# Kernel optimization log

Measured on AMD Instinct MI355X. Metric: run time of the kernel, lower is better.

The kernel has to match this reference:

```python
import jax, jax.numpy as jnp
import numpy as np

B, S, IN, OUT = 4, 2048, 4096, 1024
ROUNDS = 12  # prime_factors(4096) == [2]*12
QMIN, QMAX = -128, 127


def _create_noise(key, shape, lo, hi):
    # Obfuscation noise spanning the data range; exactly corrected in forward.
    return jax.random.uniform(key, shape, jnp.float32, -0.5, 0.5) * (hi - lo)


def setup_inputs() -> dict:
    key = jax.random.key(0)
    ks = jax.random.split(key, 6)
    x = jax.random.normal(ks[0], (B, S, IN), jnp.float32)
    weight = jax.random.normal(ks[1], (OUT, IN), jnp.float32) * 0.02
    bias = jax.random.normal(ks[2], (OUT,), jnp.float32) * 0.02
    weight_noise = _create_noise(ks[3], (OUT, IN), weight.min(), weight.max())
    noise_x = _create_noise(ks[4], (B, S, IN), x.min(), x.max())
    # one random permutation of in_features per round
    perms = jnp.stack([jax.random.permutation(jax.random.fold_in(key, 1000 + r), IN)
                       for r in range(ROUNDS)]).astype(jnp.int32)
    # 2048 random orthogonal 2x2 blocks per round (rotations, like ortho_group with dim=2)
    theta = jax.random.uniform(ks[5], (ROUNDS, IN // 2), jnp.float32, 0.0, 2.0 * np.pi)
    c, s = jnp.cos(theta), jnp.sin(theta)
    row0 = jnp.stack([c, -s], axis=-1)
    row1 = jnp.stack([s, c], axis=-1)
    matrices = jnp.stack([row0, row1], axis=-2)  # (ROUNDS, IN//2, 2, 2)
    return {"x": x, "weight": weight, "bias": bias, "weight_noise": weight_noise,
            "noise_x": noise_x, "permutations": perms, "matrices": matrices}


def _permute_matrix_operation(X, perms, mats):
    # X: (..., n, cols). Each round: gather rows by permutation, then apply a
    # block-diagonal orthogonal transform (G blocks of size f along the n axis).
    lead = X.shape[:-2]
    n, cols = X.shape[-2], X.shape[-1]
    G, f = mats.shape[1], mats.shape[2]
    for r in range(mats.shape[0]):
        X = jnp.take(X, perms[r], axis=-2)
        Xb = X.reshape(lead + (G, f, cols))
        X = jnp.einsum('gij,...gjc->...gic', mats[r], Xb).reshape(lead + (n, cols))
    return X


def _quant_dequant(t):
    # Asymmetric per-tensor quantize -> round -> clamp -> dequantize (int8-style).
    lo, hi = t.min(), t.max()
    scale = (hi - lo) / (QMAX - QMIN)
    zp = jnp.round(QMIN - lo / scale)
    q = jnp.clip(jnp.round(t / scale + zp), QMIN, QMAX)
    return (q - zp) * scale


def reference(x, weight, bias, weight_noise, noise_x, permutations, matrices):
    # inverse-transpose blocks; equals `matrices` for orthogonal blocks, kept explicit for fidelity
    inv_mats_mT = jnp.swapaxes(jnp.linalg.inv(matrices), -1, -2)
    w_plus = weight + weight_noise                                   # (OUT, IN)
    permuted_w = jnp.swapaxes(
        _permute_matrix_operation(jnp.swapaxes(w_plus, -1, -2), permutations, inv_mats_mT), -1, -2)
    qw = _quant_dequant(permuted_w)                                  # (OUT, IN)
    permuted_x = jnp.swapaxes(
        _permute_matrix_operation(jnp.swapaxes(x + noise_x, -1, -2), permutations, matrices), -1, -2)
    qx = _quant_dequant(permuted_x)                                  # (B, S, IN)
    res = qx @ qw.T + bias                                           # quantized matmul + bias
    res = res - x @ weight_noise.T                                   # correction term 1
    res = res - noise_x @ w_plus.T                                   # correction term 2
    return res
```

## Files before the change

### kernel.cpp

```cpp
#include <hip/hip_runtime.h>


#define IN_F   4096
#define OUT_F  1024
#define MROWS  8192
#define KTOT   12288
#define KHALF  6144
#define NPASS  6
#define NTIL   96

typedef _Float16 f16;
typedef _Float16 f16x8 __attribute__((ext_vector_type(8)));
typedef _Float16 f16x4 __attribute__((ext_vector_type(4)));
typedef float    f32x4 __attribute__((ext_vector_type(4)));

#define OFF_XT  (0ull)
#define OFF_WT  (OFF_XT + (size_t)MROWS * IN_F * 4)
#define OFF_A   (OFF_WT + (size_t)OUT_F * IN_F * 4)
#define OFF_B   (OFF_A + (size_t)MROWS * KTOT * 2)
#define OFF_MM  (OFF_B + (size_t)OUT_F * KTOT * 2)
#define OFF_TIX (OFF_MM + 256)
#define OFF_TCX (OFF_TIX + (size_t)NPASS * 2048 * 8)
#define OFF_TIW (OFF_TCX + (size_t)NPASS * 2048 * 32)
#define OFF_TCW (OFF_TIW + (size_t)NPASS * 2048 * 8)

__device__ __forceinline__ unsigned enc_f(float f) {
  unsigned u = __float_as_uint(f);
  return (u & 0x80000000u) ? ~u : (u | 0x80000000u);
}
__device__ __forceinline__ float dec_f(unsigned u) {
  unsigned b = (u & 0x80000000u) ? (u & 0x7fffffffu) : ~u;
  return __uint_as_float(b);
}

__global__ void build_tables_kernel(const int* __restrict__ perms,
                                    const float* __restrict__ mats,
                                    uint2* __restrict__ tIx, float4* __restrict__ tCx,
                                    uint2* __restrict__ tIw, float4* __restrict__ tCw,
                                    unsigned* __restrict__ mm) {
  if (blockIdx.x == 0 && threadIdx.x == 0) {
    mm[0] = 0xFFFFFFFFu; mm[1] = 0u; mm[2] = 0xFFFFFFFFu; mm[3] = 0u;
  }
  int p = blockIdx.x;
  int r0 = 2 * p, r1 = 2 * p + 1;
  for (int g = threadIdx.x; g < 2048; g += blockDim.x) {
    int q0 = perms[r1 * IN_F + 2 * g], q1 = perms[r1 * IN_F + 2 * g + 1];
    int a0 = q0 >> 1, e0 = q0 & 1, a1 = q1 >> 1, e1 = q1 & 1;
    unsigned i0 = perms[r0 * IN_F + 2 * a0], i1 = perms[r0 * IN_F + 2 * a0 + 1];
    unsigned i2 = perms[r0 * IN_F + 2 * a1], i3 = perms[r0 * IN_F + 2 * a1 + 1];
    uint2 idx = make_uint2(i0 | (i1 << 16), i2 | (i3 << 16));
    const float* Ma = mats + ((size_t)r0 * 2048 + a0) * 4;
    const float* Mb = mats + ((size_t)r0 * 2048 + a1) * 4;
    const float* M1 = mats + ((size_t)r1 * 2048 + g) * 4;
    int o = p * 2048 + g;
    {
      float c00 = Ma[e0 * 2], c01 = Ma[e0 * 2 + 1];
      float c10 = Mb[e1 * 2], c11 = Mb[e1 * 2 + 1];
      float m00 = M1[0], m01 = M1[1], m10 = M1[2], m11 = M1[3];
      tIx[o] = idx;
      tCx[2 * o]     = make_float4(m00 * c00, m00 * c01, m01 * c10, m01 * c11);
      tCx[2 * o + 1] = make_float4(m10 * c00, m10 * c01, m11 * c10, m11 * c11);
    }
    {
      float rda = 1.0f / (Ma[0] * Ma[3] - Ma[1] * Ma[2]);
      float rdb = 1.0f / (Mb[0] * Mb[3] - Mb[1] * Mb[2]);
      float rd1 = 1.0f / (M1[0] * M1[3] - M1[1] * M1[2]);
      float c00 = (e0 == 0 ? Ma[3] : -Ma[1]) * rda;
      float c01 = (e0 == 0 ? -Ma[2] : Ma[0]) * rda;
      float c10 = (e1 == 0 ? Mb[3] : -Mb[1]) * rdb;
      float c11 = (e1 == 0 ? -Mb[2] : Mb[0]) * rdb;
      float m00 = M1[3] * rd1, m01 = -M1[2] * rd1;
      float m10 = -M1[1] * rd1, m11 = M1[0] * rd1;
      tIw[o] = idx;
      tCw[2 * o]     = make_float4(m00 * c00, m00 * c01, m01 * c10, m01 * c11);
      tCw[2 * o + 1] = make_float4(m10 * c00, m10 * c01, m11 * c10, m11 * c11);
    }
  }
}

__global__ __launch_bounds__(1024) void transform_kernel(
    const float* __restrict__ x, const float* __restrict__ nx,
    const float* __restrict__ w, const float* __restrict__ wn,
    const uint2* __restrict__ tIx, const float4* __restrict__ tCx,
    const uint2* __restrict__ tIw, const float4* __restrict__ tCw,
    float* __restrict__ xt, float* __restrict__ wt,
    f16* __restrict__ Aall, f16* __restrict__ Ball,
    unsigned* __restrict__ mm) {
  __shared__ float2 buf[2][IN_F];
  const int t = threadIdx.x;
  const bool isW = blockIdx.x >= (MROWS / 2);
  const float *in0, *in1; const uint2* tI; const float4* tC;
  float* tout; f16* fout; int mmidx; size_t m0;
  if (!isW) {
    m0 = (size_t)blockIdx.x * 2;
    in0 = x; in1 = nx; tI = tIx; tC = tCx; tout = xt; fout = Aall; mmidx = 0;
  } else {
    m0 = (size_t)(blockIdx.x - MROWS / 2) * 2;
    in0 = w; in1 = wn; tI = tIw; tC = tCw; tout = wt; fout = Ball; mmidx = 2;
  }
  f16* f0 = fout + m0 * KTOT;
  f16* f1 = fout + (m0 + 1) * KTOT;

  {
    float4 a0 = ((const float4*)(in0 + m0 * IN_F))[t];
    float4 b0 = ((const float4*)(in1 + m0 * IN_F))[t];
    float4 a1 = ((const float4*)(in0 + (m0 + 1) * IN_F))[t];
    float4 b1 = ((const float4*)(in1 + (m0 + 1) * IN_F))[t];
    float4 s0 = make_float4(a0.x + b0.x, a0.y + b0.y, a0.z + b0.z, a0.w + b0.w);
    float4 s1 = make_float4(a1.x + b1.x, a1.y + b1.y, a1.z + b1.z, a1.w + b1.w);
    int c = t * 4;
    *(float4*)&buf[0][c]     = make_float4(s0.x, s1.x, s0.y, s1.y);
    *(float4*)&buf[0][c + 2] = make_float4(s0.z, s1.z, s0.w, s1.w);
    f16x4 p0, p1, q0, q1;
    if (isW) {
      p0.x=(f16)b0.x; p0.y=(f16)b0.y; p0.z=(f16)b0.z; p0.w=(f16)b0.w;
      q0.x=(f16)s0.x; q0.y=(f16)s0.y; q0.z=(f16)s0.z; q0.w=(f16)s0.w;
      p1.x=(f16)b1.x; p1.y=(f16)b1.y; p1.z=(f16)b1.z; p1.w=(f16)b1.w;
      q1.x=(f16)s1.x; q1.y=(f16)s1.y; q1.z=(f16)s1.z; q1.w=(f16)s1.w;
    } else {
      p0.x=(f16)(-a0.x); p0.y=(f16)(-a0.y); p0.z=(f16)(-a0.z); p0.w=(f16)(-a0.w);
      q0.x=(f16)(-b0.x); q0.y=(f16)(-b0.y); q0.z=(f16)(-b0.z); q0.w=(f16)(-b0.w);
      p1.x=(f16)(-a1.x); p1.y=(f16)(-a1.y); p1.z=(f16)(-a1.z); p1.w=(f16)(-a1.w);
      q1.x=(f16)(-b1.x); q1.y=(f16)(-b1.y); q1.z=(f16)(-b1.z); q1.w=(f16)(-b1.w);
    }
    *(f16x4*)(f0 + IN_F + c)     = p0;
    *(f16x4*)(f0 + 2 * IN_F + c) = q0;
    *(f16x4*)(f1 + IN_F + c)     = p1;
    *(f16x4*)(f1 + 2 * IN_F + c) = q1;
  }
  __syncthreads();

  int cur = 0;
  for (int pass = 0; pass < NPASS; pass++) {
    const uint2* ti = tI + pass * 2048;
    const float4* tc = tC + (size_t)pass * 4096;
#pragma unroll
    for (int i = 0; i < 2; i++) {
      int g = i * 1024 + t;
      uint2 pk = ti[g];
      float4 cA = tc[2 * g], cB = tc[2 * g + 1];
      float2 x0 = buf[cur][pk.x & 0xffff], x1 = buf[cur][pk.x >> 16];
      float2 x2 = buf[cur][pk.y & 0xffff], x3 = buf[cur][pk.y >> 16];
      float y0x = cA.x * x0.x + cA.y * x1.x + cA.z * x2.x + cA.w * x3.x;
      float y0y = cA.x * x0.y + cA.y * x1.y + cA.z * x2.y + cA.w * x3.y;
      float y1x = cB.x * x0.x + cB.y * x1.x + cB.z * x2.x + cB.w * x3.x;
      float y1y = cB.x * x0.y + cB.y * x1.y + cB.z * x2.y + cB.w * x3.y;
      *(float4*)&buf[cur ^ 1][2 * g] = make_float4(y0x, y0y, y1x, y1y);
    }
    cur ^= 1;
    __syncthreads();
  }
  float lmin = 3.4e38f, lmax = -3.4e38f;
  {
    int c = t * 4;
    float4 q0 = *(float4*)&buf[0][c];
    float4 q1 = *(float4*)&buf[0][c + 2];
    ((float4*)(tout + m0 * IN_F))[t]       = make_float4(q0.x, q0.z, q1.x, q1.z);
    ((float4*)(tout + (m0 + 1) * IN_F))[t] = make_float4(q0.y, q0.w, q1.y, q1.w);
    lmin = fminf(fminf(fminf(q0.x, q0.y), fminf(q0.z, q0.w)),
                 fminf(fminf(q1.x, q1.y), fminf(q1.z, q1.w)));
    lmax = fmaxf(fmaxf(fmaxf(q0.x, q0.y), fmaxf(q0.z, q0.w)),
                 fmaxf(fmaxf(q1.x, q1.y), fmaxf(q1.z, q1.w)));
  }
#pragma unroll
  for (int off = 32; off > 0; off >>= 1) {
    lmin = fminf(lmin, __shfl_down(lmin, off));
    lmax = fmaxf(lmax, __shfl_down(lmax, off));
  }
  float* red = (float*)&buf[1][0];
  int wid = t >> 6;
  if ((t & 63) == 0) { red[wid * 2] = lmin; red[wid * 2 + 1] = lmax; }
  __syncthreads();
  if (t == 0) {
    float bmin = red[0], bmax = red[1];
#pragma unroll
    for (int i = 1; i < 16; i++) {
      bmin = fminf(bmin, red[i * 2]);
      bmax = fmaxf(bmax, red[i * 2 + 1]);
    }
    atomicMin(&mm[mmidx], enc_f(bmin));
    atomicMax(&mm[mmidx + 1], enc_f(bmax));
  }
}

__global__ void finalize_kernel(unsigned* mm) {
  float* sc = (float*)(mm + 4);
  float xlo = dec_f(mm[0]), xhi = dec_f(mm[1]);
  float wlo = dec_f(mm[2]), whi = dec_f(mm[3]);
  float sx = (xhi - xlo) / 255.0f;
  float zx = rintf(-128.0f - xlo / sx);
  float sw = (whi - wlo) / 255.0f;
  float zw = rintf(-128.0f - wlo / sw);
  sc[0] = sx; sc[1] = zx; sc[2] = sw; sc[3] = zw;
}

__global__ __launch_bounds__(256) void quant_kernel(
    const float* __restrict__ xt, const float* __restrict__ wt,
    f16* __restrict__ Aall, f16* __restrict__ Ball,
    const unsigned* __restrict__ mm) {
  const float* sc = (const float*)(mm + 4);
  const bool isW = blockIdx.x >= MROWS;
  int m = isW ? blockIdx.x - MROWS : blockIdx.x;
  float s = isW ? sc[2] : sc[0], zp = isW ? sc[3] : sc[1];
  const float4* srow = (const float4*)((isW ? wt : xt) + (size_t)m * IN_F);
  f16* drow = (isW ? Ball : Aall) + (size_t)m * KTOT;
  int t = threadIdx.x;
#pragma unroll
  for (int j = 0; j < 4; j++) {
    int i4 = j * 256 + t;
    float4 v = srow[i4];
    float q0 = (fminf(fmaxf(rintf(v.x / s + zp), -128.f), 127.f) - zp) * s;
    float q1 = (fminf(fmaxf(rintf(v.y / s + zp), -128.f), 127.f) - zp) * s;
    float q2 = (fminf(fmaxf(rintf(v.z / s + zp), -128.f), 127.f) - zp) * s;
    float q3 = (fminf(fmaxf(rintf(v.w / s + zp), -128.f), 127.f) - zp) * s;
    f16x4 o; o.x = (f16)q0; o.y = (f16)q1; o.z = (f16)q2; o.w = (f16)q3;
    *(f16x4*)(drow + i4 * 4) = o;
  }
}

__global__ __launch_bounds__(256) void bias_init_kernel(
    const float* __restrict__ bias, float* __restrict__ out) {
  const float4* b4 = (const float4*)bias;
  float4* o4 = (float4*)out;
  int idx = blockIdx.x * 256 + threadIdx.x;
  const int total = MROWS * OUT_F / 4;
  for (int i = idx; i < total; i += gridDim.x * 256)
    o4[i] = b4[i & (OUT_F / 4 - 1)];
}

__device__ __forceinline__ void gl2lds16(const void* g, void* l) {
  __builtin_amdgcn_global_load_lds(
      (__attribute__((address_space(1))) void*)g,
      (__attribute__((address_space(3))) void*)l, 16, 0, 0);
}

#define GBAR() asm volatile("s_barrier" ::: "memory")
#define MFMA16(d, va, vb) d = __builtin_amdgcn_mfma_f32_16x16x32_f16(va, vb, d, 0, 0, 0)

#define STAGE(t, hh) do {                                                   \
    const int c_ = (t) & 1;                                                 \
    if ((hh) < 2) {                                                         \
      const f16* g_ = gA + (size_t)((hh) * 128) * KTOT + (size_t)(t) * 64;  \
      f16* l_ = As + c_ * 16384 + (hh) * 8192 + sbase;                      \
      gl2lds16(g_, l_);                                                     \
      gl2lds16(g_ + (size_t)64 * KTOT, l_ + 4096);                          \
    } else {                                                                \
      const f16* g_ = gB + (size_t)(((hh) - 2) * 128) * KTOT + (size_t)(t) * 64; \
      f16* l_ = Bs + c_ * 16384 + ((hh) - 2) * 8192 + sbase;                \
      gl2lds16(g_, l_);                                                     \
      gl2lds16(g_ + (size_t)64 * KTOT, l_ + 4096);                          \
    }                                                                       \
  } while (0)

__global__ __launch_bounds__(512, 2) void gemm_kernel(
    const f16* __restrict__ A, const f16* __restrict__ B,
    float* __restrict__ out) {
  extern __shared__ f16 sm[];
  f16* As = sm;
  f16* Bs = sm + 32768;

  const int tid = threadIdx.x;
  const int wave = tid >> 6, lane = tid & 63;
  const int fr = lane & 15, quad = lane >> 4;
  const int wm = wave >> 2, wn = wave & 3;

  const int orig = blockIdx.x;
  const int wg = (orig & 7) * 32 + (orig >> 3);
  const int ks = wg >> 7;
  const int rem = wg & 127;
  const int bn = rem >> 5, bm = rem & 31;
  const size_t k0 = (size_t)ks * KHALF;

  const int srow = (wave << 3) + (lane >> 3);
  const int scol = (((lane & 7) ^ (lane >> 3)) << 3);
  const f16* gA = A + ((size_t)bm * 256 + srow) * KTOT + k0 + scol;
  const f16* gB = B + ((size_t)bn * 256 + srow) * KTOT + k0 + scol;
  const int sbase = wave << 9;

  const int co0 = ((quad ^ (fr & 7)) << 3);
  const int co1 = co0 ^ 32;
  const f16* rA0 = As + wm * 8192 + fr * 64 + co0;
  const f16* rA1 = As + wm * 8192 + fr * 64 + co1;
  const f16* rB0 = Bs + (wn >> 1) * 8192 + (wn & 1) * 4096 + fr * 64 + co0;
  const f16* rB1 = Bs + (wn >> 1) * 8192 + (wn & 1) * 4096 + fr * 64 + co1;

  f16x8 a0[4][2], a1[4][2], bF[4][2];
  f32x4 acc[8][4] = {};

  STAGE(0, 0); STAGE(0, 1); STAGE(0, 2); STAGE(0, 3);
  STAGE(1, 0); STAGE(1, 1);
  asm volatile("s_waitcnt vmcnt(4)" ::: "memory");
  GBAR();

  for (int t = 0; t < NTIL; ++t) {
    const int c = t & 1;
    const f16* pa0 = rA0 + c * 16384;
    const f16* pa1 = rA1 + c * 16384;
    const f16* pb0 = rB0 + c * 16384;
    const f16* pb1 = rB1 + c * 16384;

#pragma unroll
    for (int i = 0; i < 4; i++) {
      a0[i][0] = *(const f16x8*)(pa0 + i * 1024);
      a0[i][1] = *(const f16x8*)(pa1 + i * 1024);
    }
#pragma unroll
    for (int j = 0; j < 2; j++) {
      bF[j][0] = *(const f16x8*)(pb0 + j * 1024);
      bF[j][1] = *(const f16x8*)(pb1 + j * 1024);
    }
    if (t + 1 < NTIL) STAGE(t + 1, 2);
    GBAR();
    __builtin_amdgcn_s_setprio(1);
#pragma unroll
    for (int i = 0; i < 4; i++)
#pragma unroll
      for (int j = 0; j < 2; j++) {
        MFMA16(acc[i][j], a0[i][0], bF[j][0]);
        MFMA16(acc[i][j], a0[i][1], bF[j][1]);
      }
    __builtin_amdgcn_s_setprio(0);
    GBAR();

#pragma unroll
    for (int i = 0; i < 4; i++) {
      a1[i][0] = *(const f16x8*)(pa0 + (4 + i) * 1024);
      a1[i][1] = *(const f16x8*)(pa1 + (4 + i) * 1024);
    }
#pragma unroll
    for (int j = 0; j < 2; j++) {
      bF[2 + j][0] = *(const f16x8*)(pb0 + (2 + j) * 1024);
      bF[2 + j][1] = *(const f16x8*)(pb1 + (2 + j) * 1024);
    }
    if (t + 1 < NTIL) STAGE(t + 1, 3);
    GBAR();
    __builtin_amdgcn_s_setprio(1);
#pragma unroll
    for (int i = 0; i < 4; i++)
#pragma unroll
      for (int j = 0; j < 2; j++) {
        MFMA16(acc[i][2 + j], a0[i][0], bF[2 + j][0]);
        MFMA16(acc[i][2 + j], a0[i][1], bF[2 + j][1]);
      }
    __builtin_amdgcn_s_setprio(0);
    GBAR();

    if (t + 2 < NTIL) STAGE(t + 2, 0);
    GBAR();
    __builtin_amdgcn_s_setprio(1);
#pragma unroll
    for (int i = 0; i < 4; i++)
#pragma unroll
      for (int j = 0; j < 2; j++) {
        MFMA16(acc[4 + i][j], a1[i][0], bF[j][0]);
        MFMA16(acc[4 + i][j], a1[i][1], bF[j][1]);
      }
    __builtin_amdgcn_s_setprio(0);
    GBAR();

    if (t + 2 < NTIL) STAGE(t + 2, 1);
    if (t + 2 < NTIL) {
      asm volatile("s_waitcnt vmcnt(4)" ::: "memory");
    } else if (t + 1 < NTIL) {
      asm volatile("s_waitcnt vmcnt(0)" ::: "memory");
    }
    GBAR();
    __builtin_amdgcn_s_setprio(1);
#pragma unroll
    for (int i = 0; i < 4; i++)
#pragma unroll
      for (int j = 0; j < 2; j++) {
        MFMA16(acc[4 + i][2 + j], a1[i][0], bF[2 + j][0]);
        MFMA16(acc[4 + i][2 + j], a1[i][1], bF[2 + j][1]);
      }
    __builtin_amdgcn_s_setprio(0);
    GBAR();
  }

  const size_t orow = (size_t)bm * 256 + wm * 128 + quad * 4;
  const int ocol = bn * 256 + wn * 64 + fr;
#pragma unroll
  for (int mi = 0; mi < 8; mi++)
#pragma unroll
    for (int ni = 0; ni < 4; ni++)
#pragma unroll
      for (int e = 0; e < 4; e++)
        unsafeAtomicAdd(&out[(orow + mi * 16 + e) * OUT_F + (ocol + ni * 16)],
                        acc[mi][ni][e]);
}

extern "C" void kernel_launch(void* const* d_in, const int* in_sizes, int n_in,
                              void* d_out, int out_size, void* d_ws, size_t ws_size,
                              hipStream_t stream) {
  const float* x     = (const float*)d_in[0];
  const float* w     = (const float*)d_in[1];
  const float* bias  = (const float*)d_in[2];
  const float* wn    = (const float*)d_in[3];
  const float* nx    = (const float*)d_in[4];
  const int*   perms = (const int*)d_in[5];
  const float* mats  = (const float*)d_in[6];
  float* out = (float*)d_out;

  char* ws = (char*)d_ws;
  float* xt   = (float*)(ws + OFF_XT);
  float* wt   = (float*)(ws + OFF_WT);
  f16*   Aall = (f16*)(ws + OFF_A);
  f16*   Ball = (f16*)(ws + OFF_B);
  unsigned* mm = (unsigned*)(ws + OFF_MM);
  uint2*  tIx = (uint2*)(ws + OFF_TIX);
  float4* tCx = (float4*)(ws + OFF_TCX);
  uint2*  tIw = (uint2*)(ws + OFF_TIW);
  float4* tCw = (float4*)(ws + OFF_TCW);

  static int attr_set = 0;
  if (!attr_set) {
    (void)hipFuncSetAttribute(reinterpret_cast<const void*>(gemm_kernel),
                              hipFuncAttributeMaxDynamicSharedMemorySize, 131072);
    attr_set = 1;
  }

  build_tables_kernel<<<NPASS, 256, 0, stream>>>(perms, mats, tIx, tCx, tIw, tCw, mm);
  transform_kernel<<<MROWS / 2 + OUT_F / 2, 1024, 0, stream>>>(
      x, nx, w, wn, tIx, tCx, tIw, tCw, xt, wt, Aall, Ball, mm);
  finalize_kernel<<<1, 1, 0, stream>>>(mm);
  quant_kernel<<<MROWS + OUT_F, 256, 0, stream>>>(xt, wt, Aall, Ball, mm);
  bias_init_kernel<<<1024, 256, 0, stream>>>(bias, out);
  gemm_kernel<<<2 * (MROWS / 256) * (OUT_F / 256), 512, 131072, stream>>>(Aall, Ball, out);
}
```

Before: 673.9 us.

## Process four rows per transform block with swizzled LDS and reschedule GEMM fragment loads

The transform kernel now handles four rows per block, holding float4 per column in a 128KB dynamic LDS buffer with an XOR swizzle. This spreads each permutation-table and coefficient load across four rows instead of two and is meant to reduce LDS bank conflicts. The quant kernel likewise processes four rows per block. In the GEMM main loop, the a1/bF fragment loads move earlier and the vmcnt wait moves after the last MFMA group, to overlap loads with compute. The larger LDS footprint lowers occupancy of the transform kernel.

```diff
diff --git a/kernel.cpp b/kernel.cpp
--- a/kernel.cpp
+++ b/kernel.cpp
@@ -24,6 +24,8 @@
 #define OFF_TIW (OFF_TCX + (size_t)NPASS * 2048 * 32)
 #define OFF_TCW (OFF_TIW + (size_t)NPASS * 2048 * 8)
 
+#define SW(s) ((s) ^ (((s) >> 3) & 7))
+
 __device__ __forceinline__ unsigned enc_f(float f) {
   unsigned u = __float_as_uint(f);
   return (u & 0x80000000u) ? ~u : (u | 0x80000000u);
@@ -31,6 +33,14 @@
 __device__ __forceinline__ float dec_f(unsigned u) {
   unsigned b = (u & 0x80000000u) ? (u & 0x7fffffffu) : ~u;
   return __uint_as_float(b);
+}
+
+__device__ __forceinline__ float4 f4comb(float4 c, float4 x0, float4 x1,
+                                         float4 x2, float4 x3) {
+  return make_float4(c.x * x0.x + c.y * x1.x + c.z * x2.x + c.w * x3.x,
+                     c.x * x0.y + c.y * x1.y + c.z * x2.y + c.w * x3.y,
+                     c.x * x0.z + c.y * x1.z + c.z * x2.z + c.w * x3.z,
+                     c.x * x0.w + c.y * x1.w + c.z * x2.w + c.w * x3.w);
 }
 
 __global__ void build_tables_kernel(const int* __restrict__ perms,
@@ -86,47 +96,54 @@
     float* __restrict__ xt, float* __restrict__ wt,
     f16* __restrict__ Aall, f16* __restrict__ Ball,
     unsigned* __restrict__ mm) {
-  __shared__ float2 buf[2][IN_F];
+  extern __shared__ float4 buf[];
   const int t = threadIdx.x;
-  const bool isW = blockIdx.x >= (MROWS / 2);
+  const bool isW = blockIdx.x >= (MROWS / 4);
   const float *in0, *in1; const uint2* tI; const float4* tC;
   float* tout; f16* fout; int mmidx; size_t m0;
   if (!isW) {
-    m0 = (size_t)blockIdx.x * 2;
+    m0 = (size_t)blockIdx.x * 4;
     in0 = x; in1 = nx; tI = tIx; tC = tCx; tout = xt; fout = Aall; mmidx = 0;
   } else {
-    m0 = (size_t)(blockIdx.x - MROWS / 2) * 2;
+    m0 = (size_t)(blockIdx.x - MROWS / 4) * 4;
     in0 = w; in1 = wn; tI = tIw; tC = tCw; tout = wt; fout = Ball; mmidx = 2;
   }
-  f16* f0 = fout + m0 * KTOT;
-  f16* f1 = fout + (m0 + 1) * KTOT;
 
   {
-    float4 a0 = ((const float4*)(in0 + m0 * IN_F))[t];
-    float4 b0 = ((const float4*)(in1 + m0 * IN_F))[t];
+    float4 a0 = ((const float4*)(in0 + (m0 + 0) * IN_F))[t];
     float4 a1 = ((const float4*)(in0 + (m0 + 1) * IN_F))[t];
+    float4 a2 = ((const float4*)(in0 + (m0 + 2) * IN_F))[t];
+    float4 a3 = ((const float4*)(in0 + (m0 + 3) * IN_F))[t];
+    float4 b0 = ((const float4*)(in1 + (m0 + 0) * IN_F))[t];
     float4 b1 = ((const float4*)(in1 + (m0 + 1) * IN_F))[t];
+    float4 b2 = ((const float4*)(in1 + (m0 + 2) * IN_F))[t];
+    float4 b3 = ((const float4*)(in1 + (m0 + 3) * IN_F))[t];
     float4 s0 = make_float4(a0.x + b0.x, a0.y + b0.y, a0.z + b0.z, a0.w + b0.w);
     float4 s1 = make_float4(a1.x + b1.x, a1.y + b1.y, a1.z + b1.z, a1.w + b1.w);
+    float4 s2 = make_float4(a2.x + b2.x, a2.y + b2.y, a2.z + b2.z, a2.w + b2.w);
+    float4 s3 = make_float4(a3.x + b3.x, a3.y + b3.y, a3.z + b3.z, a3.w + b3.w);
     int c = t * 4;
-    *(float4*)&buf[0][c]     = make_float4(s0.x, s1.x, s0.y, s1.y);
-    *(float4*)&buf[0][c + 2] = make_float4(s0.z, s1.z, s0.w, s1.w);
-    f16x4 p0, p1, q0, q1;
-    if (isW) {
-      p0.x=(f16)b0.x; p0.y=(f16)b0.y; p0.z=(f16)b0.z; p0.w=(f16)b0.w;
-      q0.x=(f16)s0.x; q0.y=(f16)s0.y; q0.z=(f16)s0.z; q0.w=(f16)s0.w;
-      p1.x=(f16)b1.x; p1.y=(f16)b1.y; p1.z=(f16)b1.z; p1.w=(f16)b1.w;
-      q1.x=(f16)s1.x; q1.y=(f16)s1.y; q1.z=(f16)s1.z; q1.w=(f16)s1.w;
-    } else {
-      p0.x=(f16)(-a0.x); p0.y=(f16)(-a0.y); p0.z=(f16)(-a0.z); p0.w=(f16)(-a0.w);
-      q0.x=(f16)(-b0.x); q0.y=(f16)(-b0.y); q0.z=(f16)(-b0.z); q0.w=(f16)(-b0.w);
-      p1.x=(f16)(-a1.x); p1.y=(f16)(-a1.y); p1.z=(f16)(-a1.z); p1.w=(f16)(-a1.w);
-      q1.x=(f16)(-b1.x); q1.y=(f16)(-b1.y); q1.z=(f16)(-b1.z); q1.w=(f16)(-b1.w);
-    }
-    *(f16x4*)(f0 + IN_F + c)     = p0;
-    *(f16x4*)(f0 + 2 * IN_F + c) = q0;
-    *(f16x4*)(f1 + IN_F + c)     = p1;
-    *(f16x4*)(f1 + 2 * IN_F + c) = q1;
+    buf[SW(c + 0)] = make_float4(s0.x, s1.x, s2.x, s3.x);
+    buf[SW(c + 1)] = make_float4(s0.y, s1.y, s2.y, s3.y);
+    buf[SW(c + 2)] = make_float4(s0.z, s1.z, s2.z, s3.z);
+    buf[SW(c + 3)] = make_float4(s0.w, s1.w, s2.w, s3.w);
+#pragma unroll
+    for (int r = 0; r < 4; r++) {
+      float4 av = r == 0 ? a0 : r == 1 ? a1 : r == 2 ? a2 : a3;
+      float4 bv = r == 0 ? b0 : r == 1 ? b1 : r == 2 ? b2 : b3;
+      float4 sv = r == 0 ? s0 : r == 1 ? s1 : r == 2 ? s2 : s3;
+      f16* fr = fout + (m0 + r) * KTOT;
+      f16x4 p, q;
+      if (isW) {
+        p.x=(f16)bv.x; p.y=(f16)bv.y; p.z=(f16)bv.z; p.w=(f16)bv.w;
+        q.x=(f16)sv.x; q.y=(f16)sv.y; q.z=(f16)sv.z; q.w=(f16)sv.w;
+      } else {
+        p.x=(f16)(-av.x); p.y=(f16)(-av.y); p.z=(f16)(-av.z); p.w=(f16)(-av.w);
+        q.x=(f16)(-bv.x); q.y=(f16)(-bv.y); q.z=(f16)(-bv.z); q.w=(f16)(-bv.w);
+      }
+      *(f16x4*)(fr + IN_F + c)     = p;
+      *(f16x4*)(fr + 2 * IN_F + c) = q;
+    }
   }
   __syncthreads();
 
@@ -134,18 +151,17 @@
   for (int pass = 0; pass < NPASS; pass++) {
     const uint2* ti = tI + pass * 2048;
     const float4* tc = tC + (size_t)pass * 4096;
+    const float4* bc = buf + cur * 4096;
+    float4* bn = buf + (cur ^ 1) * 4096;
 #pragma unroll
     for (int i = 0; i < 2; i++) {
       int g = i * 1024 + t;
       uint2 pk = ti[g];
       float4 cA = tc[2 * g], cB = tc[2 * g + 1];
-      float2 x0 = buf[cur][pk.x & 0xffff], x1 = buf[cur][pk.x >> 16];
-      float2 x2 = buf[cur][pk.y & 0xffff], x3 = buf[cur][pk.y >> 16];
-      float y0x = cA.x * x0.x + cA.y * x1.x + cA.z * x2.x + cA.w * x3.x;
-      float y0y = cA.x * x0.y + cA.y * x1.y + cA.z * x2.y + cA.w * x3.y;
-      float y1x = cB.x * x0.x + cB.y * x1.x + cB.z * x2.x + cB.w * x3.x;
-      float y1y = cB.x * x0.y + cB.y * x1.y + cB.z * x2.y + cB.w * x3.y;
-      *(float4*)&buf[cur ^ 1][2 * g] = make_float4(y0x, y0y, y1x, y1y);
+      float4 x0 = bc[SW(pk.x & 0xffff)], x1 = bc[SW(pk.x >> 16)];
+      float4 x2 = bc[SW(pk.y & 0xffff)], x3 = bc[SW(pk.y >> 16)];
+      bn[SW(2 * g)]     = f4comb(cA, x0, x1, x2, x3);
+      bn[SW(2 * g + 1)] = f4comb(cB, x0, x1, x2, x3);
     }
     cur ^= 1;
     __syncthreads();
@@ -153,21 +169,31 @@
   float lmin = 3.4e38f, lmax = -3.4e38f;
   {
     int c = t * 4;
-    float4 q0 = *(float4*)&buf[0][c];
-    float4 q1 = *(float4*)&buf[0][c + 2];
-    ((float4*)(tout + m0 * IN_F))[t]       = make_float4(q0.x, q0.z, q1.x, q1.z);
-    ((float4*)(tout + (m0 + 1) * IN_F))[t] = make_float4(q0.y, q0.w, q1.y, q1.w);
-    lmin = fminf(fminf(fminf(q0.x, q0.y), fminf(q0.z, q0.w)),
-                 fminf(fminf(q1.x, q1.y), fminf(q1.z, q1.w)));
-    lmax = fmaxf(fmaxf(fmaxf(q0.x, q0.y), fmaxf(q0.z, q0.w)),
-                 fmaxf(fmaxf(q1.x, q1.y), fmaxf(q1.z, q1.w)));
+    float4 q0 = buf[SW(c + 0)];
+    float4 q1 = buf[SW(c + 1)];
+    float4 q2 = buf[SW(c + 2)];
+    float4 q3 = buf[SW(c + 3)];
+    ((float4*)(tout + (m0 + 0) * IN_F))[t] = make_float4(q0.x, q1.x, q2.x, q3.x);
+    ((float4*)(tout + (m0 + 1) * IN_F))[t] = make_float4(q0.y, q1.y, q2.y, q3.y);
+    ((float4*)(tout + (m0 + 2) * IN_F))[t] = make_float4(q0.z, q1.z, q2.z, q3.z);
+    ((float4*)(tout + (m0 + 3) * IN_F))[t] = make_float4(q0.w, q1.w, q2.w, q3.w);
+    float mn0 = fminf(fminf(q0.x, q0.y), fminf(q0.z, q0.w));
+    float mn1 = fminf(fminf(q1.x, q1.y), fminf(q1.z, q1.w));
+    float mn2 = fminf(fminf(q2.x, q2.y), fminf(q2.z, q2.w));
+    float mn3 = fminf(fminf(q3.x, q3.y), fminf(q3.z, q3.w));
+    float mx0 = fmaxf(fmaxf(q0.x, q0.y), fmaxf(q0.z, q0.w));
+    float mx1 = fmaxf(fmaxf(q1.x, q1.y), fmaxf(q1.z, q1.w));
+    float mx2 = fmaxf(fmaxf(q2.x, q2.y), fmaxf(q2.z, q2.w));
+    float mx3 = fmaxf(fmaxf(q3.x, q3.y), fmaxf(q3.z, q3.w));
+    lmin = fminf(fminf(mn0, mn1), fminf(mn2, mn3));
+    lmax = fmaxf(fmaxf(mx0, mx1), fmaxf(mx2, mx3));
   }
 #pragma unroll
   for (int off = 32; off > 0; off >>= 1) {
     lmin = fminf(lmin, __shfl_down(lmin, off));
     lmax = fmaxf(lmax, __shfl_down(lmax, off));
   }
-  float* red = (float*)&buf[1][0];
+  float* red = (float*)(buf + 4096);
   int wid = t >> 6;
   if ((t & 63) == 0) { red[wid * 2] = lmin; red[wid * 2 + 1] = lmax; }
   __syncthreads();
@@ -199,22 +225,25 @@
     f16* __restrict__ Aall, f16* __restrict__ Ball,
     const unsigned* __restrict__ mm) {
   const float* sc = (const float*)(mm + 4);
-  const bool isW = blockIdx.x >= MROWS;
-  int m = isW ? blockIdx.x - MROWS : blockIdx.x;
+  const bool isW = blockIdx.x >= (MROWS / 4);
+  size_t m0 = (size_t)(isW ? blockIdx.x - MROWS / 4 : blockIdx.x) * 4;
   float s = isW ? sc[2] : sc[0], zp = isW ? sc[3] : sc[1];
-  const float4* srow = (const float4*)((isW ? wt : xt) + (size_t)m * IN_F);
-  f16* drow = (isW ? Ball : Aall) + (size_t)m * KTOT;
   int t = threadIdx.x;
 #pragma unroll
-  for (int j = 0; j < 4; j++) {
-    int i4 = j * 256 + t;
-    float4 v = srow[i4];
-    float q0 = (fminf(fmaxf(rintf(v.x / s + zp), -128.f), 127.f) - zp) * s;
-    float q1 = (fminf(fmaxf(rintf(v.y / s + zp), -128.f), 127.f) - zp) * s;
-    float q2 = (fminf(fmaxf(rintf(v.z / s + zp), -128.f), 127.f) - zp) * s;
-    float q3 = (fminf(fmaxf(rintf(v.w / s + zp), -128.f), 127.f) - zp) * s;
-    f16x4 o; o.x = (f16)q0; o.y = (f16)q1; o.z = (f16)q2; o.w = (f16)q3;
-    *(f16x4*)(drow + i4 * 4) = o;
+  for (int r = 0; r < 4; r++) {
+    const float4* srow = (const float4*)((isW ? wt : xt) + (m0 + r) * IN_F);
+    f16* drow = (isW ? Ball : Aall) + (m0 + r) * KTOT;
+#pragma unroll
+    for (int j = 0; j < 4; j++) {
+      int i4 = j * 256 + t;
+      float4 v = srow[i4];
+      float q0 = (fminf(fmaxf(rintf(v.x / s + zp), -128.f), 127.f) - zp) * s;
+      float q1 = (fminf(fmaxf(rintf(v.y / s + zp), -128.f), 127.f) - zp) * s;
+      float q2 = (fminf(fmaxf(rintf(v.z / s + zp), -128.f), 127.f) - zp) * s;
+      float q3 = (fminf(fmaxf(rintf(v.w / s + zp), -128.f), 127.f) - zp) * s;
+      f16x4 o; o.x = (f16)q0; o.y = (f16)q1; o.z = (f16)q2; o.w = (f16)q3;
+      *(f16x4*)(drow + i4 * 4) = o;
+    }
   }
 }
 
@@ -309,6 +338,16 @@
       bF[j][0] = *(const f16x8*)(pb0 + j * 1024);
       bF[j][1] = *(const f16x8*)(pb1 + j * 1024);
     }
+#pragma unroll
+    for (int j = 0; j < 2; j++) {
+      bF[2 + j][0] = *(const f16x8*)(pb0 + (2 + j) * 1024);
+      bF[2 + j][1] = *(const f16x8*)(pb1 + (2 + j) * 1024);
+    }
+#pragma unroll
+    for (int i = 0; i < 4; i++) {
+      a1[i][0] = *(const f16x8*)(pa0 + (4 + i) * 1024);
+      a1[i][1] = *(const f16x8*)(pa1 + (4 + i) * 1024);
+    }
     if (t + 1 < NTIL) STAGE(t + 1, 2);
     GBAR();
     __builtin_amdgcn_s_setprio(1);
@@ -322,16 +361,6 @@
     __builtin_amdgcn_s_setprio(0);
     GBAR();
 
-#pragma unroll
-    for (int i = 0; i < 4; i++) {
-      a1[i][0] = *(const f16x8*)(pa0 + (4 + i) * 1024);
-      a1[i][1] = *(const f16x8*)(pa1 + (4 + i) * 1024);
-    }
-#pragma unroll
-    for (int j = 0; j < 2; j++) {
-      bF[2 + j][0] = *(const f16x8*)(pb0 + (2 + j) * 1024);
-      bF[2 + j][1] = *(const f16x8*)(pb1 + (2 + j) * 1024);
-    }
     if (t + 1 < NTIL) STAGE(t + 1, 3);
     GBAR();
     __builtin_amdgcn_s_setprio(1);
@@ -359,11 +388,6 @@
     GBAR();
 
     if (t + 2 < NTIL) STAGE(t + 2, 1);
-    if (t + 2 < NTIL) {
-      asm volatile("s_waitcnt vmcnt(4)" ::: "memory");
-    } else if (t + 1 < NTIL) {
-      asm volatile("s_waitcnt vmcnt(0)" ::: "memory");
-    }
     GBAR();
     __builtin_amdgcn_s_setprio(1);
 #pragma unroll
@@ -374,6 +398,11 @@
         MFMA16(acc[4 + i][2 + j], a1[i][1], bF[2 + j][1]);
       }
     __builtin_amdgcn_s_setprio(0);
+    if (t + 2 < NTIL) {
+      asm volatile("s_waitcnt vmcnt(4)" ::: "memory");
+    } else if (t + 1 < NTIL) {
+      asm volatile("s_waitcnt vmcnt(0)" ::: "memory");
+    }
     GBAR();
   }
 
@@ -416,14 +445,16 @@
   if (!attr_set) {
     (void)hipFuncSetAttribute(reinterpret_cast<const void*>(gemm_kernel),
                               hipFuncAttributeMaxDynamicSharedMemorySize, 131072);
+    (void)hipFuncSetAttribute(reinterpret_cast<const void*>(transform_kernel),
+                              hipFuncAttributeMaxDynamicSharedMemorySize, 131072);
     attr_set = 1;
   }
 
   build_tables_kernel<<<NPASS, 256, 0, stream>>>(perms, mats, tIx, tCx, tIw, tCw, mm);
-  transform_kernel<<<MROWS / 2 + OUT_F / 2, 1024, 0, stream>>>(
+  transform_kernel<<<MROWS / 4 + OUT_F / 4, 1024, 131072, stream>>>(
       x, nx, w, wn, tIx, tCx, tIw, tCw, xt, wt, Aall, Ball, mm);
   finalize_kernel<<<1, 1, 0, stream>>>(mm);
-  quant_kernel<<<MROWS + OUT_F, 256, 0, stream>>>(xt, wt, Aall, Ball, mm);
+  quant_kernel<<<(MROWS + OUT_F) / 4, 256, 0, stream>>>(xt, wt, Aall, Ball, mm);
   bias_init_kernel<<<1024, 256, 0, stream>>>(bias, out);
   gemm_kernel<<<2 * (MROWS / 256) * (OUT_F / 256), 512, 131072, stream>>>(Aall, Ball, out);
 }
```

After: 684.1 us. Within noise of the previous version (+1.5%).
